# Optimization experiments

Hardware: AMD Instinct MI355X
Metric: run time of the kernel (lower is better)

Reference implementation:

```python
import jax, jax.numpy as jnp
import numpy as np

D = 64      # hidden_dim
H = 4       # num_attention_heads
DH = D // H # head_dim
B = 64      # graphs per batch
SCALE = np.float32(np.sqrt(DH))


def _sage(x, edge, wl, bl, wr):
    # SAGEConv: lin_l(mean_j x_j) + lin_r(x_i); mean over incoming edges (dst = edge[1])
    src, dst = edge[0], edge[1]
    n = x.shape[0]
    agg = jax.ops.segment_sum(x[src], dst, num_segments=n)
    cnt = jax.ops.segment_sum(jnp.ones((edge.shape[1],), x.dtype), dst, num_segments=n)
    mean = agg / jnp.maximum(cnt, 1.0)[:, None]
    return mean @ wl + bl + x @ wr


def _cross_attn(xq, xk, w, b):
    # w: [3, D, D] stacked (Q, K, V) projections; b: [3, D]
    Q = (xq @ w[0] + b[0]).reshape(-1, H, DH)  # [Nq, H, DH]
    K = (xk @ w[1] + b[1]).reshape(-1, H, DH)  # [Nk, H, DH]
    V = (xk @ w[2] + b[2]).reshape(-1, H, DH)
    scores = jnp.einsum('qhd,khd->hqk', Q, K) / SCALE  # [H, Nq, Nk]
    wgt = jax.nn.softmax(scores, axis=-1)
    out = jnp.einsum('hqk,khd->qhd', wgt, V)
    return out.reshape(xq.shape[0], D)


def _segment_mean(x, seg, num):
    s = jax.ops.segment_sum(x, seg, num_segments=num)
    c = jax.ops.segment_sum(jnp.ones((x.shape[0],), x.dtype), seg, num_segments=num)
    return s / jnp.maximum(c, 1.0)[:, None]


def setup_inputs() -> dict:
    key = jax.random.key(0)
    ks = jax.random.split(key, 32)
    N_MOL, N_PROT, E_MOL, E_PROT = 2048, 8192, 32768, 131072
    MOL_IN, PROT_IN = 32, 64

    def lin(k, i, o, s=None):
        s = 1.0 / np.sqrt(i) if s is None else s
        return (jax.random.normal(k, (i, o), jnp.float32) * s)

    inp = {
        'x_mol': jax.random.normal(ks[0], (N_MOL, MOL_IN), jnp.float32),
        'x_prot': jax.random.normal(ks[1], (N_PROT, PROT_IN), jnp.float32),
        'm1_wl': lin(ks[2], MOL_IN, D), 'm1_bl': jnp.zeros((D,), jnp.float32), 'm1_wr': lin(ks[3], MOL_IN, D),
        'm2_wl': lin(ks[4], D, D), 'm2_bl': jnp.zeros((D,), jnp.float32), 'm2_wr': lin(ks[5], D, D),
        'p1_wl': lin(ks[6], PROT_IN, D), 'p1_bl': jnp.zeros((D,), jnp.float32), 'p1_wr': lin(ks[7], PROT_IN, D),
        'p2_wl': lin(ks[8], D, D), 'p2_bl': jnp.zeros((D,), jnp.float32), 'p2_wr': lin(ks[9], D, D),
        'amp_w': jax.random.normal(ks[10], (3, D, D), jnp.float32) / np.sqrt(D),
        'amp_b': jnp.zeros((3, D), jnp.float32),
        'apm_w': jax.random.normal(ks[11], (3, D, D), jnp.float32) / np.sqrt(D),
        'apm_b': jnp.zeros((3, D), jnp.float32),
        'fc1_w': lin(ks[12], 2 * D, D), 'fc1_b': jnp.zeros((D,), jnp.float32),
        'fc2_w': lin(ks[13], D, 1), 'fc2_b': jnp.zeros((1,), jnp.float32),
        'edge_mol': jax.random.randint(ks[14], (2, E_MOL), 0, N_MOL, jnp.int32),
        'edge_prot': jax.random.randint(ks[15], (2, E_PROT), 0, N_PROT, jnp.int32),
        'batch_mol': jnp.sort(jax.random.randint(ks[16], (N_MOL,), 0, B, jnp.int32)),
        'batch_prot': jnp.sort(jax.random.randint(ks[17], (N_PROT,), 0, B, jnp.int32)),
    }
    return inp


def reference(x_mol, x_prot,
              m1_wl, m1_bl, m1_wr, m2_wl, m2_bl, m2_wr,
              p1_wl, p1_bl, p1_wr, p2_wl, p2_bl, p2_wr,
              amp_w, amp_b, apm_w, apm_b,
              fc1_w, fc1_b, fc2_w, fc2_b,
              edge_mol, edge_prot, batch_mol, batch_prot):
    # two SAGE conv blocks per graph, ReLU after each (HeteroConv with one edge type)
    h_mol = jax.nn.relu(_sage(x_mol, edge_mol, m1_wl, m1_bl, m1_wr))
    h_mol = jax.nn.relu(_sage(h_mol, edge_mol, m2_wl, m2_bl, m2_wr))
    h_prot = jax.nn.relu(_sage(x_prot, edge_prot, p1_wl, p1_bl, p1_wr))
    h_prot = jax.nn.relu(_sage(h_prot, edge_prot, p2_wl, p2_bl, p2_wr))
    # cross attention (mol queries prot, prot queries mol) + residual
    h_mol_c = h_mol + _cross_attn(h_mol, h_prot, amp_w, amp_b)
    h_prot_c = h_prot + _cross_attn(h_prot, h_mol, apm_w, apm_b)
    # global mean pool per graph
    z_mol = _segment_mean(h_mol_c, batch_mol, B)    # [B, D]
    z_prot = _segment_mean(h_prot_c, batch_prot, B)  # [B, D]
    z = jnp.concatenate([z_mol, z_prot], axis=1)     # [B, 2D]
    x = jax.nn.relu(z @ fc1_w + fc1_b)
    out = jax.nn.sigmoid(x @ fc2_w + fc2_b)
    return out.squeeze(-1)  # [B]
```

## Files before the change

### kernel.cpp

```cpp
#include <hip/hip_runtime.h>
#include <math.h>

#define D 64
#define NB 64

typedef __attribute__((ext_vector_type(8))) short bf16x8;
typedef __attribute__((ext_vector_type(4))) float f32x4;
typedef __attribute__((ext_vector_type(16))) float f32x16;

#define M3(a, b, c) fmaxf(fmaxf((a), (b)), (c))

__device__ __forceinline__ unsigned short f2bf(float f) {
    unsigned u = __float_as_uint(f);
    u += 0x7FFF + ((u >> 16) & 1);
    return (unsigned short)(u >> 16);
}
__device__ __forceinline__ unsigned pk_bf16(float lo, float hi) {
    unsigned r;
    asm("v_cvt_pk_bf16_f32 %0, %1, %2" : "=v"(r) : "v"(lo), "v"(hi));
    return r;
}
__device__ __forceinline__ float fexp2(float x) {
    float r;
    asm("v_exp_f32 %0, %1" : "=v"(r) : "v"(x));
    return r;
}

__global__ void k_prep2(const int* __restrict__ em, int Em,
                        const int* __restrict__ ep, int Ep,
                        int* __restrict__ degm, int* __restrict__ degp,
                        const int* __restrict__ bm, int Nm, int* __restrict__ bsM,
                        const int* __restrict__ bp, int Np, int* __restrict__ bsP) {
    int i = blockIdx.x * blockDim.x + threadIdx.x;
    if (i < Em) atomicAdd(&degm[em[Em + i]], 1);
    int j = i - Em;
    if (j >= 0 && j < Ep) atomicAdd(&degp[ep[Ep + j]], 1);
    if (i < Nm) {
        int cur = bm[i];
        int prev = (i == 0) ? -1 : bm[i - 1];
        for (int b = prev + 1; b <= cur; ++b) bsM[b] = i;
        if (i == Nm - 1)
            for (int b = cur + 1; b <= NB; ++b) bsM[b] = Nm;
    }
    int j2 = i - Nm;
    if (j2 >= 0 && j2 < Np) {
        int cur = bp[j2];
        int prev = (j2 == 0) ? -1 : bp[j2 - 1];
        for (int b = prev + 1; b <= cur; ++b) bsP[b] = j2;
        if (j2 == Np - 1)
            for (int b = cur + 1; b <= NB; ++b) bsP[b] = Np;
    }
}

__global__ __launch_bounds__(256) void k_scan2(
        const int* __restrict__ degm, int Nm, int* __restrict__ rpm, int* __restrict__ curm,
        const int* __restrict__ degp, int Np, int* __restrict__ rpp, int* __restrict__ curp) {
    __shared__ int sdeg[8192];
    __shared__ int chunk[256];
    const int* deg = blockIdx.x ? degp : degm;
    int N = blockIdx.x ? Np : Nm;
    int* rowptr = blockIdx.x ? rpp : rpm;
    int* cursor = blockIdx.x ? curp : curm;
    int t = threadIdx.x;
    for (int i = t; i < N; i += 256) sdeg[i] = deg[i];
    __syncthreads();
    int C = (N + 255) / 256;
    int start = t * C;
    int sum = 0;
    for (int i = 0; i < C; ++i)
        if (start + i < N) sum += sdeg[start + i];
    chunk[t] = sum;
    __syncthreads();
    for (int ofs = 1; ofs < 256; ofs <<= 1) {
        int v = (t >= ofs) ? chunk[t - ofs] : 0;
        __syncthreads();
        chunk[t] += v;
        __syncthreads();
    }
    int base = (t == 0) ? 0 : chunk[t - 1];
    for (int i = 0; i < C && start + i < N; ++i) {
        rowptr[start + i] = base;
        cursor[start + i] = base;
        base += sdeg[start + i];
    }
    if (t == 255) rowptr[N] = base;
}

__global__ void k_scatter2(const int* __restrict__ em, int Em, int* __restrict__ curm,
                           int* __restrict__ csrm,
                           const int* __restrict__ ep, int Ep, int* __restrict__ curp,
                           int* __restrict__ csrp) {
    int i = blockIdx.x * blockDim.x + threadIdx.x;
    if (i < Em) {
        int s = em[i], d = em[Em + i];
        csrm[atomicAdd(&curm[d], 1)] = s;
    }
    int j = i - Em;
    if (j >= 0 && j < Ep) {
        int s = ep[j], d = ep[Ep + j];
        csrp[atomicAdd(&curp[d], 1)] = s;
    }
}

template<int FIN>
__device__ __forceinline__ void gsage_body(
        const float* __restrict__ x, const int* __restrict__ rowptr,
        const int* __restrict__ csr, int N,
        const float* __restrict__ wl, const float* __restrict__ bl,
        const float* __restrict__ wr, float* __restrict__ out,
        int blk, float* __restrict__ swl, float* __restrict__ swr,
        float* __restrict__ sagg, float* __restrict__ sx) {
    for (int i = threadIdx.x; i < FIN * D; i += 256) { swl[i] = wl[i]; swr[i] = wr[i]; }
    int w = threadIdx.x >> 6;
    int lane = threadIdx.x & 63;
    int r = blk * 4 + w;
    if (r < N) {
        int e0 = rowptr[r], e1 = rowptr[r + 1];
        float inv = 1.0f / fmaxf((float)(e1 - e0), 1.0f);
        if (FIN == 64) {
            float a0 = 0.f, a1 = 0.f, a2 = 0.f, a3 = 0.f;
            int e = e0;
            for (; e + 3 < e1; e += 4) {
                a0 += x[(size_t)csr[e] * FIN + lane];
                a1 += x[(size_t)csr[e + 1] * FIN + lane];
                a2 += x[(size_t)csr[e + 2] * FIN + lane];
                a3 += x[(size_t)csr[e + 3] * FIN + lane];
            }
            for (; e < e1; ++e) a0 += x[(size_t)csr[e] * FIN + lane];
            sagg[w * 64 + lane] = ((a0 + a1) + (a2 + a3)) * inv;
            sx[w * 64 + lane] = x[(size_t)r * FIN + lane];
        } else {
            int f = lane & 31, half = lane >> 5;
            float a = 0.f;
            for (int e = e0 + half; e < e1; e += 2)
                a += x[(size_t)csr[e] * FIN + f];
            a += __shfl_xor(a, 32);
            if (half == 0) {
                sagg[w * 64 + f] = a * inv;
                sx[w * 64 + f] = x[(size_t)r * FIN + f];
            }
        }
    }
    __syncthreads();
    if (r >= N) return;
    int c = lane;
    float acc = bl[c];
    #pragma unroll 8
    for (int k = 0; k < FIN; ++k) {
        acc += sagg[w * 64 + k] * swl[k * D + c];
        acc += sx[w * 64 + k] * swr[k * D + c];
    }
    out[(size_t)r * D + c] = fmaxf(acc, 0.0f);
}

template<int FA, int FB>
__global__ __launch_bounds__(256) void k_gsage2(
        const float* __restrict__ xA, const int* __restrict__ rpA,
        const int* __restrict__ csrA, int NA,
        const float* __restrict__ wlA, const float* __restrict__ blA,
        const float* __restrict__ wrA, float* __restrict__ outA,
        const float* __restrict__ xB, const int* __restrict__ rpB,
        const int* __restrict__ csrB, int NB_,
        const float* __restrict__ wlB, const float* __restrict__ blB,
        const float* __restrict__ wrB, float* __restrict__ outB) {
    __shared__ float swl[64 * 64];
    __shared__ float swr[64 * 64];
    __shared__ float sagg[4 * 64];
    __shared__ float sx[4 * 64];
    int bA = NA / 4;
    if ((int)blockIdx.x < bA)
        gsage_body<FA>(xA, rpA, csrA, NA, wlA, blA, wrA, outA, blockIdx.x, swl, swr, sagg, sx);
    else
        gsage_body<FB>(xB, rpB, csrB, NB_, wlB, blB, wrB, outB, blockIdx.x - bA, swl, swr, sagg, sx);
}

__global__ __launch_bounds__(256) void k_qkv2(
        const float* __restrict__ xA, int NA, const float* __restrict__ xB, int NB_,
        const float* __restrict__ amp_w, const float* __restrict__ amp_b,
        const float* __restrict__ apm_w, const float* __restrict__ apm_b, float qs,
        unsigned short* __restrict__ QA, unsigned short* __restrict__ KA, unsigned short* __restrict__ VA,
        unsigned short* __restrict__ QB, unsigned short* __restrict__ KB, unsigned short* __restrict__ VB) {
    __shared__ float sq[D * D], sk[D * D], sv[D * D], sx[16 * D];
    int bA = NA / 16;
    const float *x, *wq, *bq, *wk, *bk, *wv, *bv;
    unsigned short *oq, *ok, *ov;
    int blk;
    if ((int)blockIdx.x < bA) {
        x = xA; blk = blockIdx.x;
        wq = amp_w;        bq = amp_b;
        wk = apm_w + 4096; bk = apm_b + 64;
        wv = apm_w + 8192; bv = apm_b + 128;
        oq = QA; ok = KA; ov = VA;
    } else {
        x = xB; blk = blockIdx.x - bA;
        wq = apm_w;        bq = apm_b;
        wk = amp_w + 4096; bk = amp_b + 64;
        wv = amp_w + 8192; bv = amp_b + 128;
        oq = QB; ok = KB; ov = VB;
    }
    for (int i = threadIdx.x; i < D * D; i += 256) { sq[i] = wq[i]; sk[i] = wk[i]; sv[i] = wv[i]; }
    int rbase = blk * 16;
    for (int i = threadIdx.x; i < 16 * D; i += 256) sx[i] = x[(size_t)rbase * D + i];
    __syncthreads();
    int c = threadIdx.x & 63;
    int r0 = (threadIdx.x >> 6) * 4;
    for (int rr = 0; rr < 4; ++rr) {
        int r = r0 + rr;
        float aq = bq[c], ak = bk[c], av = bv[c];
        #pragma unroll 8
        for (int k = 0; k < D; ++k) {
            float xv = sx[r * D + k];
            aq += xv * sq[k * D + c];
            ak += xv * sk[k * D + c];
            av += xv * sv[k * D + c];
        }
        size_t o = (size_t)(rbase + r) * D + c;
        oq[o] = f2bf(aq * qs);
        ok[o] = f2bf(ak);
        ov[o] = f2bf(av);
    }
}

__global__ void k_transp2(const unsigned short* __restrict__ inM, unsigned short* __restrict__ outM, int Nm,
                          const unsigned short* __restrict__ inP, unsigned short* __restrict__ outP, int Np) {
    __shared__ unsigned short tile[64][72];
    int bm = Nm >> 6;
    const unsigned short* in; unsigned short* out; int N;
    int blk = blockIdx.x;
    if (blk < bm) { in = inM; out = outM; N = Nm; }
    else { blk -= bm; in = inP; out = outP; N = Np; }
    int t = threadIdx.x;
    int rbase = blk * 64;
    {
        int r = t >> 2, c0 = (t & 3) * 16;
        const uint4* src = (const uint4*)(in + (size_t)(rbase + r) * 64 + c0);
        uint4 a = src[0], b = src[1];
        *(uint4*)(&tile[r][c0]) = a;
        *(uint4*)(&tile[r][c0 + 8]) = b;
    }
    __syncthreads();
    {
        int c = t >> 2, r0 = (t & 3) * 16;
        union { uint2 v2[4]; unsigned short s[16]; } u;
        #pragma unroll
        for (int i = 0; i < 16; ++i) u.s[i] = tile[r0 + i][c];
        int key0 = rbase + r0;
        int kc = key0 & ~31;
        int b16 = key0 & 16;
        unsigned short* op = out + (size_t)c * N;
        const int gmap[4] = {0, 8, 4, 12};
        #pragma unroll
        for (int b = 0; b < 4; ++b)
            *(uint2*)(op + kc + b16 + gmap[b]) = u.v2[b];
    }
    if (t < 8) {
        uint4 ones;
        ones.x = ones.y = ones.z = ones.w = 0x3F803F80u;
        *(uint4*)(out + (size_t)64 * N + rbase + t * 8) = ones;
    }
}

#define MAXTREE(cm, s0, s1)                                                   \
    {                                                                         \
        float c0 = M3(s0[0], s0[1], s0[2]);                                   \
        float c1 = M3(s0[3], s0[4], s0[5]);                                   \
        float c2 = M3(s0[6], s0[7], s0[8]);                                   \
        float c3 = M3(s0[9], s0[10], s0[11]);                                 \
        float c4 = M3(s0[12], s0[13], s0[14]);                                \
        float c5 = M3(s0[15], s1[0], s1[1]);                                  \
        float c6 = M3(s1[2], s1[3], s1[4]);                                   \
        float c7 = M3(s1[5], s1[6], s1[7]);                                   \
        float c8 = M3(s1[8], s1[9], s1[10]);                                  \
        float c9 = M3(s1[11], s1[12], s1[13]);                                \
        float ca = fmaxf(s1[14], s1[15]);                                     \
        float d0 = M3(c0, c1, c2);                                            \
        float d1 = M3(c3, c4, c5);                                            \
        float d2 = M3(c6, c7, c8);                                            \
        float d3 = M3(c9, ca, d0);                                            \
        cm = M3(d1, d2, d3);                                                  \
    }

#define PVPACK(S, KB, OA)                                                     \
    {                                                                         \
        union { unsigned u[4]; bf16x8 v; } f1, f2;                            \
        f1.u[0] = pk_bf16((S)[0], (S)[1]);   f1.u[1] = pk_bf16((S)[2], (S)[3]);  \
        f1.u[2] = pk_bf16((S)[4], (S)[5]);   f1.u[3] = pk_bf16((S)[6], (S)[7]);  \
        f2.u[0] = pk_bf16((S)[8], (S)[9]);   f2.u[1] = pk_bf16((S)[10], (S)[11]);\
        f2.u[2] = pk_bf16((S)[12], (S)[13]); f2.u[3] = pk_bf16((S)[14], (S)[15]);\
        bf16x8 vb0 = *(const bf16x8*)(vbase + (KB) + half * 8);               \
        bf16x8 vb1 = *(const bf16x8*)(vbase + (KB) + 16 + half * 8);          \
        OA = __builtin_amdgcn_mfma_f32_32x32x16_bf16(f1.v, vb0, OA, 0, 0, 0); \
        OA = __builtin_amdgcn_mfma_f32_32x32x16_bf16(f2.v, vb1, OA, 0, 0, 0); \
    }

__global__ __launch_bounds__(256) void k_attn4(
        const unsigned short* __restrict__ QmB, const unsigned short* __restrict__ KpB,
        const unsigned short* __restrict__ VpT, int Nm, int Np, int lsm,
        float* __restrict__ poM, float* __restrict__ pmM, float* __restrict__ plM,
        const unsigned short* __restrict__ QpB, const unsigned short* __restrict__ KmB,
        const unsigned short* __restrict__ VmT, int lsp,
        float* __restrict__ poP, float* __restrict__ pmP, float* __restrict__ plP) {
    const unsigned short *Q, *K, *Vt;
    int Nq, Nk, ls;
    float *po, *pm, *pl;
    if (blockIdx.y == 0) { Q = QmB; K = KpB; Vt = VpT; Nq = Nm; Nk = Np; ls = lsm; po = poM; pm = pmM; pl = plM; }
    else                 { Q = QpB; K = KmB; Vt = VmT; Nq = Np; Nk = Nm; ls = lsp; po = poP; pm = pmP; pl = plP; }
    int nqt = Nq >> 5;
    if ((int)blockIdx.x >= (nqt << ls)) return;
    const int qt = blockIdx.x >> ls;
    const int split = blockIdx.x & ((1 << ls) - 1);
    const int kchunk = Nk >> ls;
    const int h = threadIdx.x >> 6;
    const int lane = threadIdx.x & 63;
    const int cq = lane & 31;
    const int half = lane >> 5;
    const int h16 = h * 16;

    bf16x8 qb = *(const bf16x8*)(Q + ((size_t)(qt * 32 + cq) * D + h16 + half * 8));
    int drow = (cq < 16) ? (h16 + cq) : (cq == 16 ? 64 : h16 + 15);
    const unsigned short* vbase = Vt + (size_t)drow * Nk;

    f32x16 o0, o1, zro;
    #pragma unroll
    for (int i = 0; i < 16; ++i) { o0[i] = 0.f; o1[i] = 0.f; zro[i] = 0.f; }
    float m;

    const int kstart = split * kchunk;
    {
        const int kb = kstart;
        bf16x8 ka0 = *(const bf16x8*)(K + ((size_t)(kb + cq) * D + h16 + half * 8));
        bf16x8 ka1 = *(const bf16x8*)(K + ((size_t)(kb + 32 + cq) * D + h16 + half * 8));
        f32x16 s0 = __builtin_amdgcn_mfma_f32_32x32x16_bf16(ka0, qb, zro, 0, 0, 0);
        f32x16 s1 = __builtin_amdgcn_mfma_f32_32x32x16_bf16(ka1, qb, zro, 0, 0, 0);
        float cm;
        MAXTREE(cm, s0, s1);
        #pragma unroll
        for (int off = 1; off < 64; off <<= 1) cm = fmaxf(cm, __shfl_xor(cm, off));
        m = cm;
        #pragma unroll
        for (int i = 0; i < 16; ++i) { s0[i] = fexp2(s0[i] - m); s1[i] = fexp2(s1[i] - m); }
        PVPACK(s0, kb, o0)
        PVPACK(s1, kb + 32, o1)
    }
    for (int kb = kstart + 64; kb < kstart + kchunk; kb += 64) {
        bf16x8 ka0 = *(const bf16x8*)(K + ((size_t)(kb + cq) * D + h16 + half * 8));
        bf16x8 ka1 = *(const bf16x8*)(K + ((size_t)(kb + 32 + cq) * D + h16 + half * 8));
        f32x16 s0 = __builtin_amdgcn_mfma_f32_32x32x16_bf16(ka0, qb, zro, 0, 0, 0);
        f32x16 s1 = __builtin_amdgcn_mfma_f32_32x32x16_bf16(ka1, qb, zro, 0, 0, 0);
        float cm;
        MAXTREE(cm, s0, s1);
        if (__any(cm > m + 8.f)) {
            float cw = cm;
            #pragma unroll
            for (int off = 1; off < 64; off <<= 1) cw = fmaxf(cw, __shfl_xor(cw, off));
            float nm = fmaxf(cw, m);
            float sc = fexp2(m - nm);
            #pragma unroll
            for (int i = 0; i < 16; ++i) { o0[i] *= sc; o1[i] *= sc; }
            m = nm;
        }
        #pragma unroll
        for (int i = 0; i < 16; ++i) { s0[i] = fexp2(s0[i] - m); s1[i] = fexp2(s1[i] - m); }
        PVPACK(s0, kb, o0)
        PVPACK(s1, kb + 32, o1)
    }

    f32x16 o;
    #pragma unroll
    for (int i = 0; i < 16; ++i) o[i] = o0[i] + o1[i];

    size_t pbase = (size_t)split * Nq + qt * 32;
    if (half == 0)
        pm[(pbase + cq) * 4 + h] = m;
    if (cq == 16) {
        #pragma unroll
        for (int r = 0; r < 16; ++r) {
            int qr = (r & 3) + 8 * (r >> 2) + 4 * half;
            pl[(pbase + qr) * 4 + h] = o[r];
        }
    }
    if (cq < 16) {
        #pragma unroll
        for (int r = 0; r < 16; ++r) {
            int qr = (r & 3) + 8 * (r >> 2) + 4 * half;
            po[(pbase + qr) * 64 + h16 + cq] = o[r];
        }
    }
}

template<int NS>
__device__ __forceinline__ void comb_body(
        const float* __restrict__ po, const float* __restrict__ pm,
        const float* __restrict__ pl, int Nq,
        const float* __restrict__ resid, float* __restrict__ outc, int i) {
    int q = i >> 4;
    int part = i & 15;
    int d0 = part * 4;
    int h = part >> 2;
    float pmv[NS], plv[NS];
    #pragma unroll
    for (int s = 0; s < NS; ++s) pmv[s] = pm[((size_t)s * Nq + q) * 4 + h];
    #pragma unroll
    for (int s = 0; s < NS; ++s) plv[s] = pl[((size_t)s * Nq + q) * 4 + h];
    float M = pmv[0];
    #pragma unroll
    for (int s = 1; s < NS; ++s) M = fmaxf(M, pmv[s]);
    float4 O = {0.f, 0.f, 0.f, 0.f};
    float L = 0.f;
    #pragma unroll
    for (int s = 0; s < NS; ++s) {
        float wgt = fexp2(pmv[s] - M);
        float4 pv = *(const float4*)(po + ((size_t)s * Nq + q) * 64 + d0);
        O.x += pv.x * wgt; O.y += pv.y * wgt; O.z += pv.z * wgt; O.w += pv.w * wgt;
        L += plv[s] * wgt;
    }
    float invL = 1.0f / L;
    float4 rv = *(const float4*)(resid + (size_t)q * 64 + d0);
    float4 res;
    res.x = rv.x + O.x * invL;
    res.y = rv.y + O.y * invL;
    res.z = rv.z + O.z * invL;
    res.w = rv.w + O.w * invL;
    *(float4*)(outc + (size_t)q * 64 + d0) = res;
}

template<int NSM, int NSP>
__global__ void k_comb2t(
        const float* __restrict__ poM, const float* __restrict__ pmM, const float* __restrict__ plM,
        int Nm, const float* __restrict__ residM, float* __restrict__ outM,
        const float* __restrict__ poP, const float* __restrict__ pmP, const float* __restrict__ plP,
        int Np, const float* __restrict__ residP, float* __restrict__ outP) {
    int idx = blockIdx.x * blockDim.x + threadIdx.x;
    int mtot = Nm * 16;
    if (idx < mtot)
        comb_body<NSM>(poM, pmM, plM, Nm, residM, outM, idx);
    else if (idx - mtot < Np * 16)
        comb_body<NSP>(poP, pmP, plP, Np, residP, outP, idx - mtot);
}

__global__ void k_comb2(
        const float* __restrict__ poM, const float* __restrict__ pmM, const float* __restrict__ plM,
        int nsM, int Nm, const float* __restrict__ residM, float* __restrict__ outM,
        const float* __restrict__ poP, const float* __restrict__ pmP, const float* __restrict__ plP,
        int nsP, int Np, const float* __restrict__ residP, float* __restrict__ outP) {
    int idx = blockIdx.x * blockDim.x + threadIdx.x;
    const float *po, *pm, *pl, *resid;
    float* outc;
    int ns, Nq, i;
    int mtot = Nm * 64;
    if (idx < mtot) {
        po = poM; pm = pmM; pl = plM; ns = nsM; Nq = Nm; resid = residM; outc = outM; i = idx;
    } else {
        i = idx - mtot;
        if (i >= Np * 64) return;
        po = poP; pm = pmP; pl = plP; ns = nsP; Nq = Np; resid = residP; outc = outP;
    }
    int q = i >> 6, d = i & 63, h = d >> 4;
    float M = -1e30f;
    for (int s = 0; s < ns; ++s)
        M = fmaxf(M, pm[((size_t)s * Nq + q) * 4 + h]);
    float O = 0.f, L = 0.f;
    for (int s = 0; s < ns; ++s) {
        float wgt = fexp2(pm[((size_t)s * Nq + q) * 4 + h] - M);
        O += po[((size_t)s * Nq + q) * 64 + d] * wgt;
        L += pl[((size_t)s * Nq + q) * 4 + h] * wgt;
    }
    outc[i] = resid[i] + O / L;
}

__global__ __launch_bounds__(256) void k_pool2(
        const float* __restrict__ hM, const int* __restrict__ bsM,
        const float* __restrict__ hP, const int* __restrict__ bsP,
        float* __restrict__ zsum, float* __restrict__ zcnt) {
    __shared__ float red[4][64];
    int b = blockIdx.x & 63;
    int isP = blockIdx.x >> 6;
    const float* h = isP ? hP : hM;
    const int* bs = isP ? bsP : bsM;
    int colOff = isP ? 64 : 0;
    int n0 = bs[b], n1 = bs[b + 1];
    int w = threadIdx.x >> 6, c = threadIdx.x & 63;
    float acc = 0.f;
    for (int n = n0 + w; n < n1; n += 4)
        acc += h[(size_t)n * 64 + c];
    red[w][c] = acc;
    __syncthreads();
    if (w == 0) {
        float s = (red[0][c] + red[1][c]) + (red[2][c] + red[3][c]);
        zsum[b * 128 + colOff + c] = s;
        if (c == 0) zcnt[b * 2 + isP] = (float)(n1 - n0);
    }
}

__global__ __launch_bounds__(256) void k_head2(
        const float* __restrict__ zsum, const float* __restrict__ zcnt,
        const float* __restrict__ fc1w, const float* __restrict__ fc1b,
        const float* __restrict__ fc2w, const float* __restrict__ fc2b,
        float* __restrict__ out) {
    int b = blockIdx.x * 4 + (threadIdx.x >> 6);
    int c = threadIdx.x & 63;
    float inv0 = 1.0f / fmaxf(zcnt[b * 2 + 0], 1.0f);
    float inv1 = 1.0f / fmaxf(zcnt[b * 2 + 1], 1.0f);
    float acc = fc1b[c];
    #pragma unroll 8
    for (int k = 0; k < 128; ++k) {
        float zv = zsum[b * 128 + k] * (k < 64 ? inv0 : inv1);
        acc += zv * fc1w[k * 64 + c];
    }
    float v = fmaxf(acc, 0.0f) * fc2w[c];
    #pragma unroll
    for (int off = 32; off > 0; off >>= 1) v += __shfl_xor(v, off);
    if (c == 0) out[b] = 1.0f / (1.0f + __expf(-(v + fc2b[0])));
}

extern "C" void kernel_launch(void* const* d_in, const int* in_sizes, int n_in,
                              void* d_out, int out_size, void* d_ws, size_t ws_size,
                              hipStream_t stream) {
    const float* x_mol  = (const float*)d_in[0];
    const float* x_prot = (const float*)d_in[1];
    const float* m1_wl = (const float*)d_in[2];
    const float* m1_bl = (const float*)d_in[3];
    const float* m1_wr = (const float*)d_in[4];
    const float* m2_wl = (const float*)d_in[5];
    const float* m2_bl = (const float*)d_in[6];
    const float* m2_wr = (const float*)d_in[7];
    const float* p1_wl = (const float*)d_in[8];
    const float* p1_bl = (const float*)d_in[9];
    const float* p1_wr = (const float*)d_in[10];
    const float* p2_wl = (const float*)d_in[11];
    const float* p2_bl = (const float*)d_in[12];
    const float* p2_wr = (const float*)d_in[13];
    const float* amp_w = (const float*)d_in[14];
    const float* amp_b = (const float*)d_in[15];
    const float* apm_w = (const float*)d_in[16];
    const float* apm_b = (const float*)d_in[17];
    const float* fc1_w = (const float*)d_in[18];
    const float* fc1_b = (const float*)d_in[19];
    const float* fc2_w = (const float*)d_in[20];
    const float* fc2_b = (const float*)d_in[21];
    const int* edge_mol  = (const int*)d_in[22];
    const int* edge_prot = (const int*)d_in[23];
    const int* batch_mol  = (const int*)d_in[24];
    const int* batch_prot = (const int*)d_in[25];
    float* out = (float*)d_out;

    const int N_MOL  = in_sizes[0] / 32;
    const int N_PROT = in_sizes[1] / 64;
    const int E_MOL  = in_sizes[22] / 2;
    const int E_PROT = in_sizes[23] / 2;

    char* base = (char*)d_ws;
    size_t off = 0;
    auto alloc = [&](size_t bytes) -> void* {
        void* p = base + off;
        off = (off + bytes + 255) & ~(size_t)255;
        return p;
    };
    float* h_mol1   = (float*)alloc((size_t)N_MOL * D * sizeof(float));
    float* h_mol2   = (float*)alloc((size_t)N_MOL * D * sizeof(float));
    float* h_prot1  = (float*)alloc((size_t)N_PROT * D * sizeof(float));
    float* h_prot2  = (float*)alloc((size_t)N_PROT * D * sizeof(float));
    float* h_mol_c  = (float*)alloc((size_t)N_MOL * D * sizeof(float));
    float* h_prot_c = (float*)alloc((size_t)N_PROT * D * sizeof(float));
    float* zsum     = (float*)alloc((NB * 128 + NB * 2) * sizeof(float));
    float* zcnt     = zsum + NB * 128;
    unsigned short* Qm_b = (unsigned short*)alloc((size_t)N_MOL * D * 2);
    unsigned short* Km_b = (unsigned short*)alloc((size_t)N_MOL * D * 2);
    unsigned short* Vm_b = (unsigned short*)alloc((size_t)N_MOL * D * 2);
    unsigned short* Vm_t = (unsigned short*)alloc((size_t)N_MOL * (D + 1) * 2);
    unsigned short* Qp_b = (unsigned short*)alloc((size_t)N_PROT * D * 2);
    unsigned short* Kp_b = (unsigned short*)alloc((size_t)N_PROT * D * 2);
    unsigned short* Vp_b = (unsigned short*)alloc((size_t)N_PROT * D * 2);
    unsigned short* Vp_t = (unsigned short*)alloc((size_t)N_PROT * (D + 1) * 2);
    int* deg      = (int*)alloc(((size_t)N_MOL + N_PROT) * sizeof(int));
    int* deg_m    = deg;
    int* deg_p    = deg + N_MOL;
    int* rp_m     = (int*)alloc(((size_t)N_MOL + 1) * sizeof(int));
    int* cur_m    = (int*)alloc((size_t)N_MOL * sizeof(int));
    int* csr_m    = (int*)alloc((size_t)E_MOL * sizeof(int));
    int* rp_p     = (int*)alloc(((size_t)N_PROT + 1) * sizeof(int));
    int* cur_p    = (int*)alloc((size_t)N_PROT * sizeof(int));
    int* csr_p    = (int*)alloc((size_t)E_PROT * sizeof(int));
    int* bsM      = (int*)alloc((NB + 1) * sizeof(int));
    int* bsP      = (int*)alloc((NB + 1) * sizeof(int));

    int nsm = 16; while (nsm > 1 && (N_PROT % (64 * nsm))) nsm >>= 1;
    int nsp = 4;  while (nsp > 1 && (N_MOL % (64 * nsp)))  nsp >>= 1;
    int lsm = 31 - __builtin_clz(nsm);
    int lsp = 31 - __builtin_clz(nsp);
    float* poM = (float*)alloc((size_t)nsm * N_MOL * 64 * sizeof(float));
    float* pmM = (float*)alloc((size_t)nsm * N_MOL * 4 * sizeof(float));
    float* plM = (float*)alloc((size_t)nsm * N_MOL * 4 * sizeof(float));
    float* poP = (float*)alloc((size_t)nsp * N_PROT * 64 * sizeof(float));
    float* pmP = (float*)alloc((size_t)nsp * N_PROT * 4 * sizeof(float));
    float* plP = (float*)alloc((size_t)nsp * N_PROT * 4 * sizeof(float));

    const int BLK = 256;
    dim3 blk(BLK);
    const float QS = 0.25f * 1.4426950408889634f;

    hipMemsetAsync(deg, 0, ((size_t)N_MOL + N_PROT) * sizeof(int), stream);
    int Etot = E_MOL + E_PROT;
    k_prep2<<<(Etot + BLK - 1) / BLK, blk, 0, stream>>>(
        edge_mol, E_MOL, edge_prot, E_PROT, deg_m, deg_p,
        batch_mol, N_MOL, bsM, batch_prot, N_PROT, bsP);
    k_scan2<<<2, blk, 0, stream>>>(deg_m, N_MOL, rp_m, cur_m, deg_p, N_PROT, rp_p, cur_p);
    k_scatter2<<<(Etot + BLK - 1) / BLK, blk, 0, stream>>>(edge_mol, E_MOL, cur_m, csr_m,
                                                           edge_prot, E_PROT, cur_p, csr_p);

    k_gsage2<32, 64><<<N_MOL / 4 + N_PROT / 4, blk, 0, stream>>>(
        x_mol,  rp_m, csr_m, N_MOL,  m1_wl, m1_bl, m1_wr, h_mol1,
        x_prot, rp_p, csr_p, N_PROT, p1_wl, p1_bl, p1_wr, h_prot1);
    k_gsage2<64, 64><<<N_MOL / 4 + N_PROT / 4, blk, 0, stream>>>(
        h_mol1,  rp_m, csr_m, N_MOL,  m2_wl, m2_bl, m2_wr, h_mol2,
        h_prot1, rp_p, csr_p, N_PROT, p2_wl, p2_bl, p2_wr, h_prot2);

    k_qkv2<<<N_MOL / 16 + N_PROT / 16, blk, 0, stream>>>(
        h_mol2, N_MOL, h_prot2, N_PROT, amp_w, amp_b, apm_w, apm_b, QS,
        Qm_b, Km_b, Vm_b, Qp_b, Kp_b, Vp_b);

    k_transp2<<<N_MOL / 64 + N_PROT / 64, blk, 0, stream>>>(Vm_b, Vm_t, N_MOL, Vp_b, Vp_t, N_PROT);

    int gxm = (N_MOL / 32) * nsm;
    int gxp = (N_PROT / 32) * nsp;
    int gx = gxm > gxp ? gxm : gxp;
    k_attn4<<<dim3(gx, 2), blk, 0, stream>>>(
        Qm_b, Kp_b, Vp_t, N_MOL, N_PROT, lsm, poM, pmM, plM,
        Qp_b, Km_b, Vm_t, lsp, poP, pmP, plP);

    if (nsm == 16 && nsp == 4) {
        int tot = (N_MOL + N_PROT) * 16;
        k_comb2t<16, 4><<<(tot + BLK - 1) / BLK, blk, 0, stream>>>(
            poM, pmM, plM, N_MOL, h_mol2, h_mol_c,
            poP, pmP, plP, N_PROT, h_prot2, h_prot_c);
    } else {
        k_comb2<<<((N_MOL + N_PROT) * 64 + BLK - 1) / BLK, blk, 0, stream>>>(
            poM, pmM, plM, nsm, N_MOL, h_mol2, h_mol_c,
            poP, pmP, plP, nsp, N_PROT, h_prot2, h_prot_c);
    }

    k_pool2<<<128, blk, 0, stream>>>(h_mol_c, bsM, h_prot_c, bsP, zsum, zcnt);

    k_head2<<<16, blk, 0, stream>>>(zsum, zcnt, fc1_w, fc1_b, fc2_w, fc2_b, out);
}
```

Before: 177.4 us.

## Fold fixed softmax max into MFMA accumulator and drop online rescaling

Result: no change. 174.3 us (-1.8%).

```diff
diff --git a/kernel.cpp b/kernel.cpp
--- a/kernel.cpp
+++ b/kernel.cpp
@@ -280,7 +280,7 @@
         cm = M3(d1, d2, d3);                                                  \
     }
 
-#define PVPACK(S, KB, OA)                                                     \
+#define PVPACK(S, KB)                                                         \
     {                                                                         \
         union { unsigned u[4]; bf16x8 v; } f1, f2;                            \
         f1.u[0] = pk_bf16((S)[0], (S)[1]);   f1.u[1] = pk_bf16((S)[2], (S)[3]);  \
@@ -289,11 +289,13 @@
         f2.u[2] = pk_bf16((S)[12], (S)[13]); f2.u[3] = pk_bf16((S)[14], (S)[15]);\
         bf16x8 vb0 = *(const bf16x8*)(vbase + (KB) + half * 8);               \
         bf16x8 vb1 = *(const bf16x8*)(vbase + (KB) + 16 + half * 8);          \
-        OA = __builtin_amdgcn_mfma_f32_32x32x16_bf16(f1.v, vb0, OA, 0, 0, 0); \
-        OA = __builtin_amdgcn_mfma_f32_32x32x16_bf16(f2.v, vb1, OA, 0, 0, 0); \
-    }
-
-__global__ __launch_bounds__(256) void k_attn4(
+        __builtin_amdgcn_s_setprio(1);                                        \
+        o = __builtin_amdgcn_mfma_f32_32x32x16_bf16(f1.v, vb0, o, 0, 0, 0);   \
+        o = __builtin_amdgcn_mfma_f32_32x32x16_bf16(f2.v, vb1, o, 0, 0, 0);   \
+        __builtin_amdgcn_s_setprio(0);                                        \
+    }
+
+__global__ __launch_bounds__(256) void k_attn5(
         const unsigned short* __restrict__ QmB, const unsigned short* __restrict__ KpB,
         const unsigned short* __restrict__ VpT, int Nm, int Np, int lsm,
         float* __restrict__ poM, float* __restrict__ pmM, float* __restrict__ plM,
@@ -320,9 +322,9 @@
     int drow = (cq < 16) ? (h16 + cq) : (cq == 16 ? 64 : h16 + 15);
     const unsigned short* vbase = Vt + (size_t)drow * Nk;
 
-    f32x16 o0, o1, zro;
+    f32x16 o, mC;
     #pragma unroll
-    for (int i = 0; i < 16; ++i) { o0[i] = 0.f; o1[i] = 0.f; zro[i] = 0.f; }
+    for (int i = 0; i < 16; ++i) { o[i] = 0.f; mC[i] = 0.f; }
     float m;
 
     const int kstart = split * kchunk;
@@ -330,44 +332,30 @@
         const int kb = kstart;
         bf16x8 ka0 = *(const bf16x8*)(K + ((size_t)(kb + cq) * D + h16 + half * 8));
         bf16x8 ka1 = *(const bf16x8*)(K + ((size_t)(kb + 32 + cq) * D + h16 + half * 8));
-        f32x16 s0 = __builtin_amdgcn_mfma_f32_32x32x16_bf16(ka0, qb, zro, 0, 0, 0);
-        f32x16 s1 = __builtin_amdgcn_mfma_f32_32x32x16_bf16(ka1, qb, zro, 0, 0, 0);
+        f32x16 s0 = __builtin_amdgcn_mfma_f32_32x32x16_bf16(ka0, qb, mC, 0, 0, 0);
+        f32x16 s1 = __builtin_amdgcn_mfma_f32_32x32x16_bf16(ka1, qb, mC, 0, 0, 0);
         float cm;
         MAXTREE(cm, s0, s1);
         #pragma unroll
         for (int off = 1; off < 64; off <<= 1) cm = fmaxf(cm, __shfl_xor(cm, off));
         m = cm;
         #pragma unroll
-        for (int i = 0; i < 16; ++i) { s0[i] = fexp2(s0[i] - m); s1[i] = fexp2(s1[i] - m); }
-        PVPACK(s0, kb, o0)
-        PVPACK(s1, kb + 32, o1)
-    }
-    for (int kb = kstart + 64; kb < kstart + kchunk; kb += 64) {
-        bf16x8 ka0 = *(const bf16x8*)(K + ((size_t)(kb + cq) * D + h16 + half * 8));
-        bf16x8 ka1 = *(const bf16x8*)(K + ((size_t)(kb + 32 + cq) * D + h16 + half * 8));
-        f32x16 s0 = __builtin_amdgcn_mfma_f32_32x32x16_bf16(ka0, qb, zro, 0, 0, 0);
-        f32x16 s1 = __builtin_amdgcn_mfma_f32_32x32x16_bf16(ka1, qb, zro, 0, 0, 0);
-        float cm;
-        MAXTREE(cm, s0, s1);
-        if (__any(cm > m + 8.f)) {
-            float cw = cm;
-            #pragma unroll
-            for (int off = 1; off < 64; off <<= 1) cw = fmaxf(cw, __shfl_xor(cw, off));
-            float nm = fmaxf(cw, m);
-            float sc = fexp2(m - nm);
-            #pragma unroll
-            for (int i = 0; i < 16; ++i) { o0[i] *= sc; o1[i] *= sc; }
-            m = nm;
+        for (int i = 0; i < 16; ++i) {
+            s0[i] = fexp2(s0[i] - m);
+            s1[i] = fexp2(s1[i] - m);
+            mC[i] = -m;
         }
+        PVPACK(s0, kb)
+        PVPACK(s1, kb + 32)
+    }
+    #pragma unroll 2
+    for (int kb = kstart + 64; kb < kstart + kchunk; kb += 32) {
+        bf16x8 ka = *(const bf16x8*)(K + ((size_t)(kb + cq) * D + h16 + half * 8));
+        f32x16 s = __builtin_amdgcn_mfma_f32_32x32x16_bf16(ka, qb, mC, 0, 0, 0);
         #pragma unroll
-        for (int i = 0; i < 16; ++i) { s0[i] = fexp2(s0[i] - m); s1[i] = fexp2(s1[i] - m); }
-        PVPACK(s0, kb, o0)
-        PVPACK(s1, kb + 32, o1)
-    }
-
-    f32x16 o;
-    #pragma unroll
-    for (int i = 0; i < 16; ++i) o[i] = o0[i] + o1[i];
+        for (int i = 0; i < 16; ++i) s[i] = fexp2(s[i]);
+        PVPACK(s, kb)
+    }
 
     size_t pbase = (size_t)split * Nq + qt * 32;
     if (half == 0)
@@ -624,7 +612,7 @@
     int gxm = (N_MOL / 32) * nsm;
     int gxp = (N_PROT / 32) * nsp;
     int gx = gxm > gxp ? gxm : gxp;
-    k_attn4<<<dim3(gx, 2), blk, 0, stream>>>(
+    k_attn5<<<dim3(gx, 2), blk, 0, stream>>>(
         Qm_b, Kp_b, Vp_t, N_MOL, N_PROT, lsm, poM, pmM, plM,
         Qp_b, Km_b, Vm_t, lsp, poP, pmP, plP);
 
```
